# Optimization experiments

Measured on AMD Instinct MI355X. Metric: run time of the kernel, lower is better.

Reference implementation:

```python
import jax, jax.numpy as jnp
import numpy as np

E = 1024      # emb_size == hidden_size
H = 8         # n_heads
BATCH = 8
NUM = 48      # table rows
KW = 48       # table columns (keys)
L = NUM * KW  # 2304


def _mha(q_in, kv_in, length, Wq, bq, Wk, bk, Wv, bv, Wo, bo, n_heads=H):
    # q_in: (B, T, E), kv_in: (B, S, E); returns (T, B, E) per the torch layout.
    B, T, Em = q_in.shape
    S = kv_in.shape[1]
    dh = Em // n_heads
    q = (q_in @ Wq + bq).reshape(B, T, n_heads, dh).transpose(0, 2, 1, 3)
    k = (kv_in @ Wk + bk).reshape(B, S, n_heads, dh).transpose(0, 2, 1, 3)
    v = (kv_in @ Wv + bv).reshape(B, S, n_heads, dh).transpose(0, 2, 1, 3)
    scores = jnp.einsum('bhtd,bhsd->bhts', q, k) / jnp.asarray(np.sqrt(dh), q.dtype)
    mask = jnp.arange(S) < length  # memory_lengths masking
    scores = jnp.where(mask[None, None, None, :], scores, jnp.finfo(scores.dtype).min)
    attn = jax.nn.softmax(scores, axis=-1)
    out = jnp.einsum('bhts,bhsd->bhtd', attn, v).transpose(0, 2, 1, 3).reshape(B, T, Em)
    out = out @ Wo + bo
    return out.transpose(1, 0, 2)  # (T, B, E)


def setup_inputs() -> dict:
    key = jax.random.key(0)
    ks = jax.random.split(key, 24)

    def W(k, shape, s=0.03):
        return jax.random.normal(k, shape, dtype=jnp.float32) * s

    inp = {
        'emb': jax.random.normal(ks[0], (L, BATCH, E), dtype=jnp.float32),
        # col attention params
        'Wq_c': W(ks[1], (E, E)), 'bq_c': jnp.zeros((E,), jnp.float32),
        'Wk_c': W(ks[2], (E, E)), 'bk_c': jnp.zeros((E,), jnp.float32),
        'Wv_c': W(ks[3], (E, E)), 'bv_c': jnp.zeros((E,), jnp.float32),
        'Wo_c': W(ks[4], (E, E)), 'bo_c': jnp.zeros((E,), jnp.float32),
        # row attention params
        'Wq_r': W(ks[5], (E, E)), 'bq_r': jnp.zeros((E,), jnp.float32),
        'Wk_r': W(ks[6], (E, E)), 'bk_r': jnp.zeros((E,), jnp.float32),
        'Wv_r': W(ks[7], (E, E)), 'bv_r': jnp.zeros((E,), jnp.float32),
        'Wo_r': W(ks[8], (E, E)), 'bo_r': jnp.zeros((E,), jnp.float32),
        # fusion layers
        'W_gen': W(ks[9], (2 * E, E)),
        'W_mlp1': W(ks[10], (2 * E, E)),
        'W_mlp2': W(ks[11], (E, 1)),
        # scalar forward args
        'start_id': 0, 'end_id': L - 1,
        'num': NUM, 'num_tensor': NUM,
        'kw_num': KW, 'kw_num_tensor': KW,
        'batch': BATCH,
    }
    return inp


def reference(emb, Wq_c, bq_c, Wk_c, bk_c, Wv_c, bv_c, Wo_c, bo_c,
              Wq_r, bq_r, Wk_r, bk_r, Wv_r, bv_r, Wo_r, bo_r,
              W_gen, W_mlp1, W_mlp2,
              start_id, end_id, num, num_tensor, kw_num, kw_num_tensor, batch):
    Em = emb.shape[-1]
    length = end_id - start_id + 1  # = num * kw_num
    # emb.narrow(0, start_id, length): (L, batch, E)
    rep = emb[start_id:start_id + length]
    # -> (kw_num, batch*num, E)
    home_ply_rep = rep.transpose(1, 0, 2).reshape(batch * num, kw_num, Em).transpose(1, 0, 2)

    # --- column-dim encoding: attention over the `num` (row) axis ---
    col_mb = jnp.swapaxes(home_ply_rep.reshape(kw_num, batch, num, Em), 0, 2)  # (num, batch, kw, E)
    col_mb = col_mb.reshape(num, batch * kw_num, Em)
    col_q = col_mb.transpose(1, 0, 2)  # (batch*kw, num, E)
    col_rep = _mha(col_q, col_q, num_tensor, Wq_c, bq_c, Wk_c, bk_c, Wv_c, bv_c, Wo_c, bo_c)
    # (num, batch*kw, E) -> (kw_num, batch*num, E)
    col_dim_rep = jnp.swapaxes(col_rep.reshape(num, batch, kw_num, Em), 0, 2).reshape(kw_num, batch * num, Em)

    # --- row-dim encoding: attention over the `kw_num` (column) axis ---
    row_q = col_dim_rep.transpose(1, 0, 2)  # (batch*num, kw, E)
    row_dim_rep = _mha(row_q, row_q, kw_num_tensor, Wq_r, bq_r, Wk_r, bk_r, Wv_r, bv_r, Wo_r, bo_r)  # (kw, b*n, E)

    # --- fusion: concat + Linear + tanh, MLP scores, softmax over {row, col} ---
    gen_rep = jnp.tanh(jnp.concatenate([row_dim_rep, col_dim_rep], axis=-1) @ W_gen)

    def mlp_score(x):
        return jnp.tanh(jnp.concatenate([x, gen_rep], axis=-1) @ W_mlp1) @ W_mlp2  # (kw, b*n, 1)

    row_score = mlp_score(row_dim_rep)
    col_score = mlp_score(col_dim_rep)
    w = jax.nn.softmax(jnp.concatenate([row_score, col_score], axis=-1), axis=-1)  # (kw, b*n, 2)
    home_ply_memory_bank = w[..., 0:1] * row_dim_rep + w[..., 1:2] * col_dim_rep
    # no_fusion=True -> residual add
    home_ply_memory_bank = home_ply_memory_bank + home_ply_rep

    row_for_ptr = row_dim_rep.reshape(kw_num, batch, num, Em)
    col_for_ptr = col_dim_rep.reshape(kw_num, batch, num, Em)

    # row_aggregation == 'mean'
    home_ply_row_rep = home_ply_memory_bank.mean(axis=0)  # (batch*num, E)
    home_ply_row_rep = home_ply_row_rep.reshape(batch, num, Em).transpose(1, 0, 2)  # (num, batch, E)
    return (home_ply_row_rep, home_ply_memory_bank, col_for_ptr, row_for_ptr)
```

## Files before the change

kernel.cpp:

```cpp
#include <hip/hip_runtime.h>
#include <hip/hip_bf16.h>
#include <stdint.h>

typedef unsigned short u16;
typedef unsigned int   u32;
typedef __attribute__((ext_vector_type(4))) float f32x4;
typedef __attribute__((ext_vector_type(2))) float f32x2;
typedef __attribute__((ext_vector_type(8))) short s16x8;

#define DEV __device__ __forceinline__

static constexpr int EDIM  = 1024;
static constexpr int MROWS = 8 * 48 * 48;

DEV float b2f(u16 x) { u32 u = ((u32)x) << 16; float f; __builtin_memcpy(&f, &u, 4); return f; }
DEV u16 f2b(float f) {
    u32 u; __builtin_memcpy(&u, &f, 4);
    u32 r = (u + 0x7FFFu + ((u >> 16) & 1u)) >> 16;
    return (u16)r;
}

#define GLDS16(gsrc, ldst) __builtin_amdgcn_global_load_lds( \
    (const __attribute__((address_space(1))) u32*)(gsrc),    \
    (__attribute__((address_space(3))) u32*)(ldst), 16, 0, 0)

enum { F_WRC = 1, F_PERM = 2, F_TANH = 4, F_SCORE = 8, F_OMAP1 = 16, F_OMAP2 = 32,
       F_OUTFLIN = 64, F_HGEN = 128 };

struct GJob {
    const u16* A1; const u16* A2; const u16* Bt; const float* bias;
    u16* C; float* outF; const float* w2; float* score;
    int ldc, M, flags, tileEnd;
};
struct GSet3 { int njobs, pad; GJob j[3]; };

struct WJob { const float* src; u16* dst; int srcN, dstLd, kOff, nT, tileEnd, pad; };
struct WSet { int n, total; WJob j[12]; };

__global__ void wconvJ_kernel(WSet ws) {
    int bid = blockIdx.x;
    int ji = 0;
    while (bid >= ws.j[ji].tileEnd) ++ji;
    int base = ji ? ws.j[ji - 1].tileEnd : 0;
    WJob J = ws.j[ji];
    int lt = bid - base;
    int n0 = (lt % J.nT) * 64, k0 = (lt / J.nT) * 64;
    __shared__ u16 tile[64][65];
    int tx = threadIdx.x & 63, ty = threadIdx.x >> 6;
#pragma unroll
    for (int i = 0; i < 16; ++i) {
        int r = ty * 16 + i;
        tile[r][tx] = f2b(J.src[(size_t)(k0 + r) * J.srcN + n0 + tx]);
    }
    __syncthreads();
#pragma unroll
    for (int i = 0; i < 16; ++i) {
        int r = ty * 16 + i;
        J.dst[(size_t)(n0 + r) * J.dstLd + J.kOff + k0 + tx] = tile[tx][r];
    }
}

__global__ void misc_kernel(const float* WoCsrc, const float* WoRsrc,
                            u16* WoCnt, u16* WoRnt,
                            const float* bq_c, const float* bk_c, const float* bv_c, float* bqkvC,
                            const float* bq_r, const float* bk_r, const float* bv_r,
                            const float* bo_c, const u16* WqkvRT, float* bqkvR_eff,
                            const float* bo_r, const u16* WgaT, float* bgen_lin,
                            float* scores) {
    int id = blockIdx.x * 256 + threadIdx.x;
    const int C1 = 1024 * 1024 / 2;
    if (id < C1) {
        f32x2 v = *(const f32x2*)&WoCsrc[(size_t)id * 2];
        *(u32*)&WoCnt[(size_t)id * 2] = (u32)f2b(v.x) | ((u32)f2b(v.y) << 16);
        return;
    }
    id -= C1;
    if (id < C1) {
        f32x2 v = *(const f32x2*)&WoRsrc[(size_t)id * 2];
        *(u32*)&WoRnt[(size_t)id * 2] = (u32)f2b(v.x) | ((u32)f2b(v.y) << 16);
        return;
    }
    id -= C1;
    if (id < 3072) { bqkvC[id] = (id < 1024) ? bq_c[id] : (id < 2048) ? bk_c[id - 1024] : bv_c[id - 2048]; return; }
    id -= 3072;
    if (id < 2 * MROWS) { scores[id] = 0.f; return; }
    id -= 2 * MROWS;
    if (id < 3072) {
        float s = (id < 1024) ? bq_r[id] : (id < 2048) ? bk_r[id - 1024] : bv_r[id - 2048];
        float d = 0.f;
        const u16* row = &WqkvRT[(size_t)id * 1024];
        for (int e = 0; e < 1024; e += 8) {
            s16x8 v = *(const s16x8*)&row[e];
#pragma unroll
            for (int u = 0; u < 8; ++u) d += bo_c[e + u] * b2f((u16)v[u]);
        }
        bqkvR_eff[id] = s + d;
        return;
    }
    id -= 3072;
    if (id < 1024) {
        float d = 0.f;
        const u16* row = &WgaT[(size_t)id * 1024];
        for (int e = 0; e < 1024; e += 8) {
            s16x8 v = *(const s16x8*)&row[e];
#pragma unroll
            for (int u = 0; u < 8; ++u) d += bo_r[e + u] * b2f((u16)v[u]);
        }
        bgen_lin[id] = d;
    }
}

__global__ void gather_kernel(const float* __restrict__ emb, u16* __restrict__ Xc) {
    int gid = blockIdx.x * 256 + threadIdx.x;
    int r = gid >> 9, c2 = gid & 511;
    int b = r / 2304, k = (r / 48) % 48, n = r % 48;
    int src = (n * 48 + k) * 8 + b;
    f32x2 v = *(const f32x2*)&emb[(size_t)src * EDIM + c2 * 2];
    *(u32*)&Xc[(size_t)r * EDIM + c2 * 2] = (u32)f2b(v.x) | ((u32)f2b(v.y) << 16);
}

template<int LDA, int KT, bool DUAL, int LDA2>
DEV void gemm_core(const GJob& J, int lt) {
    extern __shared__ u16 smem[];
    u16* lA = smem;
    u16* lB = smem + 8192;
    constexpr int NT = KT / 32;

    int mtl = J.M >> 7;
    int mt = lt % mtl, nt = lt / mtl;
    int m0 = mt * 128, n0 = nt * 128;
    int tid = threadIdx.x, lane = tid & 63, wv = tid >> 6;
    int wm = wv >> 1, wn = wv & 1;
    int fr = lane & 15, qq = lane >> 4;

    int c0 = wv * 2, c1 = c0 + 1;
    int r0 = c0 * 16 + (lane >> 2), r1 = c1 * 16 + (lane >> 2);
    int qg0 = ((lane & 3) - (r0 >> 1)) & 3, qg1 = ((lane & 3) - (r1 >> 1)) & 3;
    const u16* gA0 = J.A1 + (size_t)(m0 + r0) * LDA + qg0 * 8;
    const u16* gA1 = J.A1 + (size_t)(m0 + r1) * LDA + qg1 * 8;
    const u16* gA0b = nullptr; const u16* gA1b = nullptr;
    if constexpr (DUAL) {
        gA0b = J.A2 + (size_t)(m0 + r0) * LDA2 + qg0 * 8;
        gA1b = J.A2 + (size_t)(m0 + r1) * LDA2 + qg1 * 8;
    }
    const u16* gB0 = J.Bt + (size_t)(n0 + r0) * KT + qg0 * 8;
    const u16* gB1 = J.Bt + (size_t)(n0 + r1) * KT + qg1 * 8;
    u16* dA0 = lA + c0 * 512;
    u16* dA1 = lA + c1 * 512;
    u16* dB0 = lB + c0 * 512;
    u16* dB1 = lB + c1 * 512;

    const u16* aP[4]; const u16* bP[4];
#pragma unroll
    for (int mf = 0; mf < 4; ++mf) {
        int rr = wm * 64 + mf * 16 + fr;
        aP[mf] = lA + rr * 32 + (((qq + (rr >> 1)) & 3) * 8);
        int rn = wn * 64 + mf * 16 + fr;
        bP[mf] = lB + rn * 32 + (((qq + (rn >> 1)) & 3) * 8);
    }

    f32x4 acc[4][4];
#pragma unroll
    for (int i = 0; i < 4; ++i)
#pragma unroll
        for (int jj = 0; jj < 4; ++jj) acc[i][jj] = (f32x4)0.f;

    auto STAGE = [&](int bsel, int kt) {
        int bo = bsel * 4096;
        if (DUAL && kt >= 32) {
            GLDS16(gA0b + (kt - 32) * 32, dA0 + bo);
            GLDS16(gA1b + (kt - 32) * 32, dA1 + bo);
        } else {
            GLDS16(gA0 + kt * 32, dA0 + bo);
            GLDS16(gA1 + kt * 32, dA1 + bo);
        }
        GLDS16(gB0 + kt * 32, dB0 + bo);
        GLDS16(gB1 + kt * 32, dB1 + bo);
    };

    STAGE(0, 0);
#pragma unroll
    for (int kt = 0; kt < NT; ++kt) {
        __syncthreads();
        if (kt + 1 < NT) STAGE((kt + 1) & 1, kt + 1);
        const int po = (kt & 1) * 4096;
        s16x8 af[4], bf[4];
#pragma unroll
        for (int mf = 0; mf < 4; ++mf) af[mf] = *(const s16x8*)(aP[mf] + po);
#pragma unroll
        for (int nf = 0; nf < 4; ++nf) bf[nf] = *(const s16x8*)(bP[nf] + po);
#pragma unroll
        for (int mf = 0; mf < 4; ++mf)
#pragma unroll
            for (int nf = 0; nf < 4; ++nf)
                acc[mf][nf] = __builtin_amdgcn_mfma_f32_16x16x32_bf16(af[mf], bf[nf], acc[mf][nf], 0, 0, 0);
    }

    int crow4 = qq * 4;
#pragma unroll
    for (int mf = 0; mf < 4; ++mf) {
#pragma unroll
        for (int jj = 0; jj < 4; ++jj) {
            int row = m0 + wm * 64 + mf * 16 + crow4 + jj;
            int orow = row, o32 = 0;
            if (J.flags & (F_PERM | F_OMAP1)) {
                int b = row / 2304, k = (row / 48) % 48, n = row % 48;
                if (J.flags & F_PERM)  orow = (b * 48 + n) * 48 + k;
                if (J.flags & F_OMAP1) o32 = k * 384 + b * 48 + n;
            }
            if (J.flags & F_OMAP2) {
                int b = row / 2304, n = (row / 48) % 48, k = row % 48;
                o32 = k * 384 + b * 48 + n;
            }
            float sc = 0.f;
#pragma unroll
            for (int nf = 0; nf < 4; ++nf) {
                int col = n0 + wn * 64 + nf * 16 + fr;
                float v = acc[mf][nf][jj];
                if (J.bias) v += J.bias[col];
                if (J.flags & F_HGEN) v += J.outF[(size_t)row * EDIM + col];
                if (J.flags & F_TANH) v = tanhf(v);
                if (J.flags & F_WRC) J.C[(size_t)orow * J.ldc + col] = f2b(v);
                if (J.flags & (F_OMAP1 | F_OMAP2)) J.outF[(size_t)o32 * EDIM + col] = v;
                if (J.flags & F_OUTFLIN) J.outF[(size_t)row * EDIM + col] = v;
                if (J.flags & F_SCORE) sc += v * J.w2[col];
            }
            if (J.flags & F_SCORE) {
                sc += __shfl_xor(sc, 1);
                sc += __shfl_xor(sc, 2);
                sc += __shfl_xor(sc, 4);
                sc += __shfl_xor(sc, 8);
                if (fr == 0) atomicAdd(&J.score[row], sc);
            }
        }
    }
}

template<int LDA, int KT, bool DUAL, int LDA2>
__global__ __launch_bounds__(256, 4) void gemmT_kernel(GSet3 js) {
    int bid = blockIdx.x;
    int ji = 0, base = 0;
    if (js.njobs > 1 && bid >= js.j[0].tileEnd) { ji = 1; base = js.j[0].tileEnd; }
    if (js.njobs > 2 && bid >= js.j[1].tileEnd) { ji = 2; base = js.j[1].tileEnd; }
    gemm_core<LDA, KT, DUAL, LDA2>(js.j[ji], bid - base);
}

__global__ __launch_bounds__(256, 4) void gemmD3_kernel(GJob a, GJob b, int aTiles) {
    int bid = blockIdx.x;
    if (bid < aTiles) gemm_core<3072, 1024, false, 0>(a, bid);
    else              gemm_core<3072, 2048, true, 1024>(b, bid - aTiles);
}

__global__ __launch_bounds__(64) void attn_kernel(u16* __restrict__ QKV) {
    __shared__ u16 lVt[128 * 72];
    __shared__ u16 lP[48 * 72];
    const int LDQ = 3072;
    int bb = blockIdx.x >> 3, h = blockIdx.x & 7;
    int lane = threadIdx.x;
    u16* Qp = QKV + (size_t)bb * 48 * LDQ + h * 128;
    const u16* Kp = Qp + 1024;
    const u16* Vp = Qp + 2048;

#pragma unroll
    for (int i = 0; i < 48; ++i) {
        u32 vv = *(const u32*)&Vp[(size_t)i * LDQ + lane * 2];
        lVt[(lane * 2) * 72 + i]     = (u16)(vv & 0xffffu);
        lVt[(lane * 2 + 1) * 72 + i] = (u16)(vv >> 16);
    }
    for (int i = lane; i < 128 * 16; i += 64) { int d = i >> 4, c = 48 + (i & 15); lVt[d * 72 + c] = 0; }
    for (int i = lane; i < 48 * 16; i += 64)  { int t = i >> 4, c = 48 + (i & 15); lP[t * 72 + c] = 0; }
    __syncthreads();

    int fr = lane & 15, fk = (lane >> 4) * 8, crow4 = (lane >> 4) * 4;
    f32x4 sc[3][3];
#pragma unroll
    for (int mf = 0; mf < 3; ++mf)
#pragma unroll
        for (int nf = 0; nf < 3; ++nf) sc[mf][nf] = (f32x4)0.f;

#pragma unroll
    for (int kk = 0; kk < 4; ++kk) {
        s16x8 aq[3], bk[3];
#pragma unroll
        for (int mf = 0; mf < 3; ++mf) aq[mf] = *(const s16x8*)&Qp[(size_t)(mf * 16 + fr) * LDQ + kk * 32 + fk];
#pragma unroll
        for (int nf = 0; nf < 3; ++nf) bk[nf] = *(const s16x8*)&Kp[(size_t)(nf * 16 + fr) * LDQ + kk * 32 + fk];
#pragma unroll
        for (int mf = 0; mf < 3; ++mf)
#pragma unroll
            for (int nf = 0; nf < 3; ++nf)
                sc[mf][nf] = __builtin_amdgcn_mfma_f32_16x16x32_bf16(aq[mf], bk[nf], sc[mf][nf], 0, 0, 0);
    }

    const float scale = 0.08838834764831845f;
#pragma unroll
    for (int mf = 0; mf < 3; ++mf) {
#pragma unroll
        for (int j = 0; j < 4; ++j) {
            float v0 = sc[mf][0][j] * scale;
            float v1 = sc[mf][1][j] * scale;
            float v2 = sc[mf][2][j] * scale;
            float mx = fmaxf(v0, fmaxf(v1, v2));
            mx = fmaxf(mx, __shfl_xor(mx, 1));
            mx = fmaxf(mx, __shfl_xor(mx, 2));
            mx = fmaxf(mx, __shfl_xor(mx, 4));
            mx = fmaxf(mx, __shfl_xor(mx, 8));
            float e0 = __expf(v0 - mx), e1 = __expf(v1 - mx), e2 = __expf(v2 - mx);
            float s = e0 + e1 + e2;
            s += __shfl_xor(s, 1);
            s += __shfl_xor(s, 2);
            s += __shfl_xor(s, 4);
            s += __shfl_xor(s, 8);
            float inv = 1.f / s;
            int t = mf * 16 + crow4 + j;
            lP[t * 72 + 0  + fr] = f2b(e0 * inv);
            lP[t * 72 + 16 + fr] = f2b(e1 * inv);
            lP[t * 72 + 32 + fr] = f2b(e2 * inv);
        }
    }
    __syncthreads();

    f32x4 o[3][8];
#pragma unroll
    for (int mf = 0; mf < 3; ++mf)
#pragma unroll
        for (int nf = 0; nf < 8; ++nf) o[mf][nf] = (f32x4)0.f;

#pragma unroll
    for (int kk = 0; kk < 2; ++kk) {
        s16x8 ap[3];
#pragma unroll
        for (int mf = 0; mf < 3; ++mf) ap[mf] = *(const s16x8*)&lP[(mf * 16 + fr) * 72 + kk * 32 + fk];
#pragma unroll
        for (int nf = 0; nf < 8; ++nf) {
            s16x8 bv = *(const s16x8*)&lVt[(nf * 16 + fr) * 72 + kk * 32 + fk];
#pragma unroll
            for (int mf = 0; mf < 3; ++mf)
                o[mf][nf] = __builtin_amdgcn_mfma_f32_16x16x32_bf16(ap[mf], bv, o[mf][nf], 0, 0, 0);
        }
    }
#pragma unroll
    for (int mf = 0; mf < 3; ++mf)
#pragma unroll
        for (int nf = 0; nf < 8; ++nf)
#pragma unroll
            for (int j = 0; j < 4; ++j) {
                int t = mf * 16 + crow4 + j, d = nf * 16 + fr;
                Qp[(size_t)t * LDQ + d] = f2b(o[mf][nf][j]);
            }
}

__global__ void combine_mean_kernel(const u16* __restrict__ RDR, const u16* __restrict__ CDR,
                                    const float* __restrict__ srow, const float* __restrict__ scol,
                                    const float* __restrict__ emb, float* __restrict__ out) {
    int b = blockIdx.x / 48, n = blockIdx.x % 48;
    __shared__ float w0s[48], w1s[48];
    int tx = threadIdx.x;
    if (tx < 48) {
        int r2 = (b * 48 + n) * 48 + tx;
        float rs = srow[r2], cs = scol[r2];
        float m = fmaxf(rs, cs);
        float e0 = __expf(rs - m), e1 = __expf(cs - m);
        float inv = 1.f / (e0 + e1);
        w0s[tx] = e0 * inv; w1s[tx] = e1 * inv;
    }
    __syncthreads();
    float* out_mb = out + 393216;
    for (int e = tx; e < EDIM; e += 256) {
        float s = 0.f;
        for (int k = 0; k < 48; ++k) {
            size_t rb = (size_t)((b * 48 + n) * 48 + k) * EDIM;
            float rv = b2f(RDR[rb + e]);
            float cv = b2f(CDR[rb + e]);
            float hv = emb[((size_t)(n * 48 + k) * 8 + b) * EDIM + e];
            float v = w0s[k] * rv + w1s[k] * cv + hv;
            out_mb[(size_t)(k * 384 + b * 48 + n) * EDIM + e] = v;
            s += v;
        }
        out[(size_t)(n * 8 + b) * EDIM + e] = s * (1.f / 48.f);
    }
}

extern "C" void kernel_launch(void* const* d_in, const int* in_sizes, int n_in,
                              void* d_out, int out_size, void* d_ws, size_t ws_size,
                              hipStream_t stream) {
    const float* emb    = (const float*)d_in[0];
    const float* Wq_c   = (const float*)d_in[1];
    const float* bq_c   = (const float*)d_in[2];
    const float* Wk_c   = (const float*)d_in[3];
    const float* bk_c   = (const float*)d_in[4];
    const float* Wv_c   = (const float*)d_in[5];
    const float* bv_c   = (const float*)d_in[6];
    const float* Wo_c   = (const float*)d_in[7];
    const float* bo_c   = (const float*)d_in[8];
    const float* Wq_r   = (const float*)d_in[9];
    const float* bq_r   = (const float*)d_in[10];
    const float* Wk_r   = (const float*)d_in[11];
    const float* bk_r   = (const float*)d_in[12];
    const float* Wv_r   = (const float*)d_in[13];
    const float* bv_r   = (const float*)d_in[14];
    const float* Wo_r   = (const float*)d_in[15];
    const float* bo_r   = (const float*)d_in[16];
    const float* W_gen  = (const float*)d_in[17];
    const float* W_mlp1 = (const float*)d_in[18];
    const float* W_mlp2 = (const float*)d_in[19];
    (void)in_sizes; (void)n_in; (void)out_size; (void)ws_size;

    char* ws = (char*)d_ws;
    size_t off = 0;
    auto alloc = [&](size_t bytes) { char* p = ws + off; off += (bytes + 255) & ~(size_t)255; return p; };
    u16*   WqkvCT = (u16*)alloc((size_t)3072 * 1024 * 2);
    u16*   WqkvRT = (u16*)alloc((size_t)3072 * 1024 * 2);
    u16*   WoCT   = (u16*)alloc((size_t)1024 * 1024 * 2);
    u16*   WoRT   = (u16*)alloc((size_t)1024 * 1024 * 2);
    u16*   WoCnt  = (u16*)alloc((size_t)1024 * 1024 * 2);
    u16*   WoRnt  = (u16*)alloc((size_t)1024 * 1024 * 2);
    u16*   WgaT   = (u16*)alloc((size_t)1024 * 1024 * 2);
    u16*   BtGf   = (u16*)alloc((size_t)1024 * 2048 * 2);
    u16*   W1aT   = (u16*)alloc((size_t)1024 * 1024 * 2);
    u16*   W1bT   = (u16*)alloc((size_t)1024 * 1024 * 2);
    u16*   BtQKVr = (u16*)alloc((size_t)3072 * 1024 * 2);
    float* bqkvC  = (float*)alloc(3072 * 4);
    float* bqkvRe = (float*)alloc(3072 * 4);
    float* bgen   = (float*)alloc(1024 * 4);
    u16*   XA     = (u16*)alloc((size_t)MROWS * 1024 * 2);
    u16*   QKV    = (u16*)alloc((size_t)MROWS * 3072 * 2);
    u16*   QKV2   = (u16*)alloc((size_t)MROWS * 3072 * 2);
    u16*   CDR    = (u16*)alloc((size_t)MROWS * 1024 * 2);
    u16*   RDR    = (u16*)alloc((size_t)MROWS * 1024 * 2);
    float* score_row = (float*)alloc((size_t)MROWS * 4);
    float* score_col = (float*)alloc((size_t)MROWS * 4);
    float* Hgen = (float*)QKV;

    float* out = (float*)d_out;
    float* out_col = out + 393216 + 18874368;
    float* out_row = out + 393216 + 2 * 18874368;

    dim3 tb(256);
    const int SMEM = 32768;

    WSet wset = {};
    int te = 0;
    auto addW = [&](const float* src, u16* dst, int srcN, int dstLd, int kOff, int nT, int kT) {
        int i = wset.n++;
        te += nT * kT;
        WJob w = {src, dst, srcN, dstLd, kOff, nT, te, 0};
        wset.j[i] = w;
    };
    addW(Wq_c, WqkvCT,                   1024, 1024, 0, 16, 16);
    addW(Wk_c, WqkvCT + 1024 * 1024,     1024, 1024, 0, 16, 16);
    addW(Wv_c, WqkvCT + 2 * 1024 * 1024, 1024, 1024, 0, 16, 16);
    addW(Wo_c, WoCT,                     1024, 1024, 0, 16, 16);
    addW(Wq_r, WqkvRT,                   1024, 1024, 0, 16, 16);
    addW(Wk_r, WqkvRT + 1024 * 1024,     1024, 1024, 0, 16, 16);
    addW(Wv_r, WqkvRT + 2 * 1024 * 1024, 1024, 1024, 0, 16, 16);
    addW(Wo_r, WoRT,                     1024, 1024, 0, 16, 16);
    addW(W_gen,               WgaT,      1024, 1024, 0, 16, 16);
    addW(W_gen + 1024 * 1024, BtGf,      1024, 2048, 1024, 16, 16);
    addW(W_mlp1,               W1aT,     1024, 1024, 0, 16, 16);
    addW(W_mlp1 + 1024 * 1024, W1bT,     1024, 1024, 0, 16, 16);
    wset.total = te;
    wconvJ_kernel<<<te, tb, 0, stream>>>(wset);

    int miscItems = 1024 * 1024 + 3072 + 2 * MROWS + 3072 + 1024;
    misc_kernel<<<(miscItems + 255) / 256, tb, 0, stream>>>(
        Wo_c, Wo_r, WoCnt, WoRnt,
        bq_c, bk_c, bv_c, bqkvC,
        bq_r, bk_r, bv_r,
        bo_c, WqkvRT, bqkvRe,
        bo_r, WgaT, bgen,
        score_row);

    gather_kernel<<<MROWS * 512 / 256, tb, 0, stream>>>(emb, XA);

    auto mkJob = [](const u16* A1, const u16* A2, const u16* Bt, const float* bias,
                    u16* C, float* outF, const float* w2, float* score,
                    int ldc, int M, int flags) {
        GJob j = {A1, A2, Bt, bias, C, outF, w2, score, ldc, M, flags, 0};
        return j;
    };
    auto mkset = [](GJob a, int nA, const GJob* b, int nB, const GJob* c, int nC, int& tot) {
        GSet3 gs = {};
        a.tileEnd = (a.M >> 7) * nA;
        gs.j[0] = a; tot = a.tileEnd; gs.njobs = 1;
        if (b) { GJob jb = *b; jb.tileEnd = tot + (jb.M >> 7) * nB; tot = jb.tileEnd; gs.j[1] = jb; gs.njobs = 2; }
        if (c) { GJob jc = *c; jc.tileEnd = tot + (jc.M >> 7) * nC; tot = jc.tileEnd; gs.j[2] = jc; gs.njobs = 3; }
        return gs;
    };

    {
        GJob b = mkJob(WqkvRT, nullptr, WoCnt, nullptr, BtQKVr, nullptr, nullptr, nullptr,
                       1024, 3072, F_WRC);
        GJob c = mkJob(WgaT, nullptr, WoRnt, nullptr, BtGf, nullptr, nullptr, nullptr,
                       2048, 1024, F_WRC);
        int tot;
        GSet3 gs = mkset(mkJob(XA, nullptr, WqkvCT, bqkvC, QKV, nullptr, nullptr, nullptr,
                               3072, MROWS, F_WRC), 24, &b, 8, &c, 8, tot);
        gemmT_kernel<1024, 1024, false, 0><<<tot, tb, SMEM, stream>>>(gs);
    }
    attn_kernel<<<384 * 8, 64, 0, stream>>>(QKV);
    {
        GJob b = mkJob(QKV, nullptr, BtQKVr, bqkvRe, QKV2, nullptr, nullptr, nullptr,
                       3072, MROWS, F_WRC | F_PERM);
        int tot;
        GSet3 gs = mkset(mkJob(QKV, nullptr, WoCT, bo_c, CDR, out_col, nullptr, nullptr,
                               1024, MROWS, F_WRC | F_PERM | F_OMAP1), 8, &b, 24, nullptr, 0, tot);
        gemmT_kernel<3072, 1024, false, 0><<<tot, tb, SMEM, stream>>>(gs);
    }
    attn_kernel<<<384 * 8, 64, 0, stream>>>(QKV2);
    {
        GJob a = mkJob(QKV2, nullptr, WoRT, bo_r, RDR, out_row, nullptr, nullptr,
                       1024, MROWS, F_WRC | F_OMAP2);
        GJob b = mkJob(QKV2, CDR, BtGf, bgen, XA, nullptr, nullptr, nullptr,
                       1024, MROWS, F_WRC | F_TANH);
        int aT = (MROWS >> 7) * 8;
        int bT = (MROWS >> 7) * 8;
        gemmD3_kernel<<<aT + bT, tb, SMEM, stream>>>(a, b, aT);
    }
    {
        int tot;
        GSet3 gs = mkset(mkJob(XA, nullptr, W1bT, nullptr, nullptr, Hgen, nullptr, nullptr,
                               1024, MROWS, F_OUTFLIN), 8, nullptr, 0, nullptr, 0, tot);
        gemmT_kernel<1024, 1024, false, 0><<<tot, tb, SMEM, stream>>>(gs);
    }
    {
        GJob b = mkJob(CDR, nullptr, W1aT, nullptr, nullptr, Hgen, W_mlp2, score_col,
                       1024, MROWS, F_SCORE | F_TANH | F_HGEN);
        int tot;
        GSet3 gs = mkset(mkJob(RDR, nullptr, W1aT, nullptr, nullptr, Hgen, W_mlp2, score_row,
                               1024, MROWS, F_SCORE | F_TANH | F_HGEN), 8, &b, 8, nullptr, 0, tot);
        gemmT_kernel<1024, 1024, false, 0><<<tot, tb, SMEM, stream>>>(gs);
    }

    combine_mean_kernel<<<384, tb, 0, stream>>>(RDR, CDR, score_row, score_col, emb, out);
}
```

Baseline: 1.134 ms.

## Triple-buffer GEMM LDS staging and write attention output to compact buffer

The GEMM main loop moves from double to triple buffering in LDS. It prefetches two k-tiles ahead and uses explicit vmcnt waits plus a raw s_barrier in place of __syncthreads, so global-to-LDS loads overlap more MFMA work. Shared memory per block grows to 48KB and launch bounds drop to 3 blocks per CU, which may lower occupancy. Separately, attention now writes its output to a dense 1024-wide buffer instead of overwriting Q inside the 3072-stride QKV, so the downstream GEMMs read A with a contiguous stride of 1024.

New measurement: 1.168 ms. +3.0%, slower.

```diff
diff --git a/kernel.cpp b/kernel.cpp
--- a/kernel.cpp
+++ b/kernel.cpp
@@ -123,7 +123,7 @@
 DEV void gemm_core(const GJob& J, int lt) {
     extern __shared__ u16 smem[];
     u16* lA = smem;
-    u16* lB = smem + 8192;
+    u16* lB = smem + 12288;
     constexpr int NT = KT / 32;
 
     int mtl = J.M >> 7;
@@ -179,11 +179,15 @@
     };
 
     STAGE(0, 0);
+    STAGE(1, 1);
 #pragma unroll
     for (int kt = 0; kt < NT; ++kt) {
-        __syncthreads();
-        if (kt + 1 < NT) STAGE((kt + 1) & 1, kt + 1);
-        const int po = (kt & 1) * 4096;
+        if (kt + 1 < NT) asm volatile("s_waitcnt vmcnt(4)" ::: "memory");
+        else             asm volatile("s_waitcnt vmcnt(0)" ::: "memory");
+        __builtin_amdgcn_s_barrier();
+        __builtin_amdgcn_sched_barrier(0);
+        if (kt + 2 < NT) STAGE((kt + 2) % 3, kt + 2);
+        const int po = (kt % 3) * 4096;
         s16x8 af[4], bf[4];
 #pragma unroll
         for (int mf = 0; mf < 4; ++mf) af[mf] = *(const s16x8*)(aP[mf] + po);
@@ -237,7 +241,7 @@
 }
 
 template<int LDA, int KT, bool DUAL, int LDA2>
-__global__ __launch_bounds__(256, 4) void gemmT_kernel(GSet3 js) {
+__global__ __launch_bounds__(256, 3) void gemmT_kernel(GSet3 js) {
     int bid = blockIdx.x;
     int ji = 0, base = 0;
     if (js.njobs > 1 && bid >= js.j[0].tileEnd) { ji = 1; base = js.j[0].tileEnd; }
@@ -245,21 +249,23 @@
     gemm_core<LDA, KT, DUAL, LDA2>(js.j[ji], bid - base);
 }
 
-__global__ __launch_bounds__(256, 4) void gemmD3_kernel(GJob a, GJob b, int aTiles) {
+__global__ __launch_bounds__(256, 3) void gemmD3_kernel(GJob a, GJob b, int aTiles) {
     int bid = blockIdx.x;
-    if (bid < aTiles) gemm_core<3072, 1024, false, 0>(a, bid);
-    else              gemm_core<3072, 2048, true, 1024>(b, bid - aTiles);
-}
-
-__global__ __launch_bounds__(64) void attn_kernel(u16* __restrict__ QKV) {
+    if (bid < aTiles) gemm_core<1024, 1024, false, 0>(a, bid);
+    else              gemm_core<1024, 2048, true, 1024>(b, bid - aTiles);
+}
+
+__global__ __launch_bounds__(64) void attn_kernel(const u16* __restrict__ QKV,
+                                                  u16* __restrict__ O) {
     __shared__ u16 lVt[128 * 72];
     __shared__ u16 lP[48 * 72];
     const int LDQ = 3072;
     int bb = blockIdx.x >> 3, h = blockIdx.x & 7;
     int lane = threadIdx.x;
-    u16* Qp = QKV + (size_t)bb * 48 * LDQ + h * 128;
+    const u16* Qp = QKV + (size_t)bb * 48 * LDQ + h * 128;
     const u16* Kp = Qp + 1024;
     const u16* Vp = Qp + 2048;
+    u16* Op = O + (size_t)bb * 48 * 1024 + h * 128;
 
 #pragma unroll
     for (int i = 0; i < 48; ++i) {
@@ -346,7 +352,7 @@
 #pragma unroll
             for (int j = 0; j < 4; ++j) {
                 int t = mf * 16 + crow4 + j, d = nf * 16 + fr;
-                Qp[(size_t)t * LDQ + d] = f2b(o[mf][nf][j]);
+                Op[(size_t)t * 1024 + d] = f2b(o[mf][nf][j]);
             }
 }
 
@@ -424,6 +430,7 @@
     float* bqkvRe = (float*)alloc(3072 * 4);
     float* bgen   = (float*)alloc(1024 * 4);
     u16*   XA     = (u16*)alloc((size_t)MROWS * 1024 * 2);
+    u16*   XO     = (u16*)alloc((size_t)MROWS * 1024 * 2);
     u16*   QKV    = (u16*)alloc((size_t)MROWS * 3072 * 2);
     u16*   QKV2   = (u16*)alloc((size_t)MROWS * 3072 * 2);
     u16*   CDR    = (u16*)alloc((size_t)MROWS * 1024 * 2);
@@ -437,7 +444,7 @@
     float* out_row = out + 393216 + 2 * 18874368;
 
     dim3 tb(256);
-    const int SMEM = 32768;
+    const int SMEM = 49152;
 
     WSet wset = {};
     int te = 0;
@@ -498,20 +505,20 @@
                                3072, MROWS, F_WRC), 24, &b, 8, &c, 8, tot);
         gemmT_kernel<1024, 1024, false, 0><<<tot, tb, SMEM, stream>>>(gs);
     }
-    attn_kernel<<<384 * 8, 64, 0, stream>>>(QKV);
+    attn_kernel<<<384 * 8, 64, 0, stream>>>(QKV, XO);
     {
-        GJob b = mkJob(QKV, nullptr, BtQKVr, bqkvRe, QKV2, nullptr, nullptr, nullptr,
+        GJob b = mkJob(XO, nullptr, BtQKVr, bqkvRe, QKV2, nullptr, nullptr, nullptr,
                        3072, MROWS, F_WRC | F_PERM);
         int tot;
-        GSet3 gs = mkset(mkJob(QKV, nullptr, WoCT, bo_c, CDR, out_col, nullptr, nullptr,
+        GSet3 gs = mkset(mkJob(XO, nullptr, WoCT, bo_c, CDR, out_col, nullptr, nullptr,
                                1024, MROWS, F_WRC | F_PERM | F_OMAP1), 8, &b, 24, nullptr, 0, tot);
-        gemmT_kernel<3072, 1024, false, 0><<<tot, tb, SMEM, stream>>>(gs);
-    }
-    attn_kernel<<<384 * 8, 64, 0, stream>>>(QKV2);
+        gemmT_kernel<1024, 1024, false, 0><<<tot, tb, SMEM, stream>>>(gs);
+    }
+    attn_kernel<<<384 * 8, 64, 0, stream>>>(QKV2, XO);
     {
-        GJob a = mkJob(QKV2, nullptr, WoRT, bo_r, RDR, out_row, nullptr, nullptr,
+        GJob a = mkJob(XO, nullptr, WoRT, bo_r, RDR, out_row, nullptr, nullptr,
                        1024, MROWS, F_WRC | F_OMAP2);
-        GJob b = mkJob(QKV2, CDR, BtGf, bgen, XA, nullptr, nullptr, nullptr,
+        GJob b = mkJob(XO, CDR, BtGf, bgen, XA, nullptr, nullptr, nullptr,
                        1024, MROWS, F_WRC | F_TANH);
         int aT = (MROWS >> 7) * 8;
         int bT = (MROWS >> 7) * 8;
```
